# Performance work log

Hardware: AMD Instinct MI355X
Metric: run time of the kernel (lower is better)

Reference implementation:

```python
import jax, jax.numpy as jnp
import numpy as np

N = 10000            # nodes
E = 320000           # edges (avg degree 32)
L = 4                # layers
S = 64               # hidden 0e multiplicity
V = 16               # hidden 1o multiplicity
EMB = 32             # node-attr embedding dim
NB = 8               # bessel basis per channel (r and v -> 2*NB edge feats)
MR = 2.5             # max_radius
DEG = 32.0           # num_neighbors
GS = S + V           # gate input scalars: 64 scalars + 16 gates
NW = S * 2 + V * 2 + V * 2   # 192 per-edge tensor-product weights
MAXT = 100           # max atom types


def _semi_unitary(K):
    # Newton-Schulz orthogonalization: K^T K -> I (semi-unitary uplift matrix)
    K = K / jnp.linalg.norm(K)
    for _ in range(10):
        K = 1.5 * K - 0.5 * K @ (K.T @ K)
    return K


def _smooth_cutoff(t):
    u = 2.0 * (t - 1.0)
    y = (1.0 - jnp.cos(jnp.pi * u)) * 0.5
    return jnp.where(u > 0, 0.0, jnp.where(u < -1.0, 1.0, y))


def _edge_geom(d):
    # d: (E,3) edge vector. Returns cutoff-weighted 1x1o SH (component norm) and bessel features.
    r = jnp.linalg.norm(d, axis=1)                       # (E,)
    sh = np.sqrt(3.0) * d / r[:, None]                   # spherical harmonics 1x1o
    attr = _smooth_cutoff(r / MR)[:, None] * sh          # (E,3)
    k = jnp.arange(1, NB + 1, dtype=jnp.float32) * jnp.pi
    feat = np.sqrt(2.0 / MR) * jnp.sin(k * (r / MR)[:, None]) / r[:, None]
    return attr, feat * np.sqrt(NB)                      # (E,3), (E,NB)


def _fctp(s, v, attr, Ws, Wv):
    # FullyConnectedTensorProduct with pure-scalar (0e) node attr == attr-weighted per-irrep linear
    os = jnp.einsum('ni,ne,oie->no', s, attr, Ws) / np.sqrt(s.shape[1] * EMB)
    ov = jnp.einsum('nim,ne,oie->nom', v, attr, Wv) / np.sqrt(v.shape[1] * EMB)
    return os, ov


def _forward(x, node_attr, edge_src, edge_dst, emb_table, PU_K, h, mix,
             si_Ws, si_Wv, sc_Ws, sc_Wv, lin1_Ws, lin1_Wv, lin2_Ws, lin2_Wv,
             fc_W1, fc_b1, fc_W2, fc_b2, fc_W3, fc_b3):
    attr = emb_table[node_attr]                          # (N,EMB)
    K = _semi_unitary(PU_K)                              # (V,2)
    yv = jnp.einsum('ui,nim->num', K, x.reshape(N, 2, 3))  # uplift vectors
    ys = jnp.zeros((N, S), x.dtype)
    ys_old, yv_old = ys, yv
    c_s, c_x = np.sin(np.pi / 8), np.cos(np.pi / 8)
    for i in range(L):
        ar, fr = _edge_geom(x[:, :3][edge_src] - x[:, :3][edge_dst])
        av, fv = _edge_geom(x[:, 3:][edge_src] - x[:, 3:][edge_dst])
        a = jnp.stack([ar, av], axis=1)                  # (E,2,3) = 2x1o edge attr
        ef = jnp.concatenate([fr, fv], axis=1)           # (E,2*NB)
        # radial MLP -> per-edge TP weights
        hd = jax.nn.silu(ef @ fc_W1[i] + fc_b1[i])
        hd = jax.nn.silu(hd @ fc_W2[i] + fc_b2[i])
        w = hd @ fc_W3[i] + fc_b3[i]                     # (E,NW)
        w1 = w[:, :S * 2].reshape(-1, S, 2)
        w2 = w[:, S * 2:S * 2 + V * 2].reshape(-1, V, 2)
        w3 = w[:, S * 2 + V * 2:].reshape(-1, V, 2)
        # conv: lin1 -> gather -> TP -> scatter -> lin2 ; plus self-connection
        fs, fvv = _fctp(ys, yv, attr, lin1_Ws[i], lin1_Wv[i])
        s_src, v_src = fs[edge_src], fvv[edge_src]
        # 0e x 1o -> 1o (uvu)
        o1 = jnp.einsum('euv,eu,evm->eum', w1, s_src, a) / np.sqrt(2.0)   # (E,S,3)
        # 1o x 1o -> 0e (uvu)
        dots = jnp.einsum('eum,evm->euv', v_src, a)
        o2 = jnp.einsum('euv,euv->eu', w2, dots) / np.sqrt(6.0)           # (E,V)
        # 1o x 1o -> 1o (cross, uvu)
        cr = jnp.cross(v_src[:, :, None, :], a[:, None, :, :])            # (E,V,2,3)
        o3 = jnp.einsum('euv,euvm->eum', w3, cr) / 2.0                    # (E,V,3)
        mid_s = jax.ops.segment_sum(o2, edge_dst, num_segments=N) / np.sqrt(DEG)
        mid_v = jax.ops.segment_sum(jnp.concatenate([o1, o3], axis=1), edge_dst,
                                    num_segments=N) / np.sqrt(DEG)        # (N,S+V,3)
        cs2, cv2 = _fctp(mid_s, mid_v, attr, lin2_Ws[i], lin2_Wv[i])      # (N,GS),(N,V,3)
        scs, scv = _fctp(ys, yv, attr, sc_Ws[i], sc_Wv[i])
        conv_s = c_s * scs + c_x * cs2
        conv_v = c_s * scv + c_x * cv2
        # gate: silu scalars, sigmoid gates * gated vectors
        gns = jax.nn.silu(conv_s[:, :S])
        gnv = jax.nn.sigmoid(conv_s[:, S:])[:, :, None] * conv_v
        # self-interaction: per-irrep linear
        sis = ys @ si_Ws[i].T / np.sqrt(S)
        siv = jnp.einsum('oi,nim->nom', si_Wv[i], yv) / np.sqrt(V)
        # leapfrog update
        h2 = h[i] ** 2
        ns = 2.0 * ys - ys_old + h2 * (mix[i] * gns + (mix[i] - 1.0) * sis)
        nv = 2.0 * yv - yv_old + h2 * (mix[i] * gnv + (mix[i] - 1.0) * siv)
        ys_old, yv_old = ys, yv
        ys, yv = ns, nv
        x = jnp.einsum('ui,num->nim', K, yv).reshape(N, 6)   # project
    return x


def setup_inputs() -> dict:
    key = jax.random.key(0)
    ks = jax.random.split(key, 24)
    def g(i, sh, fan=1.0):
        return jax.random.normal(ks[i], sh, dtype=jnp.float32) / np.sqrt(fan)
    edge_src = jax.random.randint(ks[20], (E,), 0, N, dtype=jnp.int32)
    off = jax.random.randint(ks[21], (E,), 1, N, dtype=jnp.int32)
    edge_dst = (edge_src + off) % N                      # guarantees src != dst
    return {
        'x': g(0, (N, 6)),
        'batch': jnp.zeros((N,), jnp.int32),
        'node_attr': jax.random.randint(ks[22], (N,), 0, MAXT, dtype=jnp.int32),
        'edge_src': edge_src,
        'edge_dst': edge_dst,
        'emb_table': g(1, (MAXT, EMB)),
        'PU_K': g(2, (V, 2)),
        'h': jnp.full((L,), 0.01, jnp.float32),
        'mix': jnp.full((L,), 0.5, jnp.float32),
        'si_Ws': g(3, (L, S, S)), 'si_Wv': g(4, (L, V, V)),
        'sc_Ws': g(5, (L, GS, S, EMB)), 'sc_Wv': g(6, (L, V, V, EMB)),
        'lin1_Ws': g(7, (L, S, S, EMB)), 'lin1_Wv': g(8, (L, V, V, EMB)),
        'lin2_Ws': g(9, (L, GS, V, EMB)), 'lin2_Wv': g(10, (L, V, S + V, EMB)),
        'fc_W1': g(11, (L, 2 * NB, 64), 2 * NB), 'fc_b1': jnp.zeros((L, 64), jnp.float32),
        'fc_W2': g(12, (L, 64, 64), 64), 'fc_b2': jnp.zeros((L, 64), jnp.float32),
        'fc_W3': g(13, (L, 64, NW), 64), 'fc_b3': jnp.zeros((L, NW), jnp.float32),
    }


def reference(x, batch, node_attr, edge_src, edge_dst, emb_table, PU_K, h, mix,
              si_Ws, si_Wv, sc_Ws, sc_Wv, lin1_Ws, lin1_Wv, lin2_Ws, lin2_Wv,
              fc_W1, fc_b1, fc_W2, fc_b2, fc_W3, fc_b3):
    return _forward(x, node_attr, edge_src, edge_dst, emb_table, PU_K, h, mix,
                    si_Ws, si_Wv, sc_Ws, sc_Wv, lin1_Ws, lin1_Wv, lin2_Ws, lin2_Wv,
                    fc_W1, fc_b1, fc_W2, fc_b2, fc_W3, fc_b3)
```

## Files before the change

kernel.cpp:

```cpp
#include <hip/hip_runtime.h>
#include <hip/hip_fp8.h>
#include <math.h>

#define NN 10000
#define NE 320000
#define PI_F 3.14159265358979323846f

typedef __attribute__((ext_vector_type(8))) short short8x;
typedef __attribute__((ext_vector_type(4))) float float4x;
typedef __attribute__((ext_vector_type(4))) unsigned short ushort4x;

#if defined(__has_builtin)
#if __has_builtin(__builtin_amdgcn_cvt_pk_fp8_f32) && __has_builtin(__builtin_amdgcn_cvt_f32_fp8)
#define HW_FP8 1
#endif
#endif

__device__ __forceinline__ unsigned short f2b(float f) {
    unsigned b = __float_as_uint(f);
    return (unsigned short)((b + 0x7FFFu + ((b >> 16) & 1u)) >> 16);
}
__device__ __forceinline__ float b2f(unsigned short u) {
    return __uint_as_float(((unsigned)u) << 16);
}
__device__ __forceinline__ float silu(float x) {
    return x / (1.f + __expf(-x));
}
__device__ __forceinline__ unsigned char f2e4(float f) {
#ifdef HW_FP8
    int r = __builtin_amdgcn_cvt_pk_fp8_f32(f, f, 0, false);
    return (unsigned char)(r & 0xff);
#else
    __hip_fp8_e4m3 q(f);
    return (unsigned char)q.__x;
#endif
}
__device__ __forceinline__ float e42f(unsigned char v) {
#ifdef HW_FP8
    return __builtin_amdgcn_cvt_f32_fp8((int)v, 0);
#else
    __hip_fp8_e4m3 q;
    q.__x = (__hip_fp8_storage_t)v;
    return (float)q;
#endif
}
__device__ __forceinline__ float e4sel(unsigned word, int sel) {
#ifdef HW_FP8
    switch (sel & 3) {
        case 0:  return __builtin_amdgcn_cvt_f32_fp8((int)word, 0);
        case 1:  return __builtin_amdgcn_cvt_f32_fp8((int)word, 1);
        case 2:  return __builtin_amdgcn_cvt_f32_fp8((int)word, 2);
        default: return __builtin_amdgcn_cvt_f32_fp8((int)word, 3);
    }
#else
    return e42f((unsigned char)((word >> (8*(sel & 3))) & 0xffu));
#endif
}
__device__ __forceinline__ unsigned pk4(float a, float b, float c, float d) {
#ifdef HW_FP8
    unsigned w = (unsigned)__builtin_amdgcn_cvt_pk_fp8_f32(a, b, 0, false);
    w = (unsigned)__builtin_amdgcn_cvt_pk_fp8_f32(c, d, (int)w, true);
    return w;
#else
    return (unsigned)f2e4(a) | ((unsigned)f2e4(b) << 8) |
           ((unsigned)f2e4(c) << 16) | ((unsigned)f2e4(d) << 24);
#endif
}

__global__ void k_newton_kernel(const float* __restrict__ PU, float* __restrict__ Kout)
{
    if (threadIdx.x != 0 || blockIdx.x != 0) return;
    float K[32];
    float nrm = 0.f;
    for (int i = 0; i < 32; ++i) { K[i] = PU[i]; nrm += K[i]*K[i]; }
    float inv = 1.0f / sqrtf(nrm);
    for (int i = 0; i < 32; ++i) K[i] *= inv;
    for (int it = 0; it < 10; ++it) {
        float m00 = 0.f, m01 = 0.f, m11 = 0.f;
        for (int u = 0; u < 16; ++u) {
            float a = K[2*u], b = K[2*u+1];
            m00 += a*a; m01 += a*b; m11 += b*b;
        }
        for (int u = 0; u < 16; ++u) {
            float a = K[2*u], b = K[2*u+1];
            K[2*u]   = 1.5f*a - 0.5f*(a*m00 + b*m01);
            K[2*u+1] = 1.5f*b - 0.5f*(a*m01 + b*m11);
        }
    }
    for (int i = 0; i < 32; ++i) Kout[i] = K[i];
}

__global__ __launch_bounds__(256) void init_all_kernel(
    const float* __restrict__ x, const float* __restrict__ K,
    float* __restrict__ xp, float* __restrict__ yv0, float* __restrict__ yv1,
    float* __restrict__ ys0, float* __restrict__ ys1, float* __restrict__ fsb)
{
    int tid = blockIdx.x*256 + threadIdx.x;
    if (tid < NN*8) {
        int n = tid >> 3, c = tid & 7;
        xp[tid] = (c < 6) ? x[n*6 + c] : 0.f;
        return;
    }
    int t2 = tid - NN*8;
    if (t2 < NN*48) {
        int n = t2/48, j = t2%48, u = j/3, m = j%3;
        float v = K[2*u]*x[n*6+m] + K[2*u+1]*x[n*6+3+m];
        yv0[t2] = v; yv1[t2] = v;
        return;
    }
    t2 -= NN*48;
    if (t2 < NN*64) { ys0[t2] = 0.f; ys1[t2] = 0.f; fsb[t2] = 0.f; }
}

__global__ void init_fvv_kernel(const float* __restrict__ yv, const int* __restrict__ types,
                                const float* __restrict__ lin1vT0, float* __restrict__ fvv)
{
    int tid = blockIdx.x*blockDim.x + threadIdx.x;
    if (tid >= NN*48) return;
    int n = tid/48, j = tid%48, o = j/3, m = j%3;
    int t = types[n];
    const float* W = lin1vT0 + (size_t)t*256;
    float acc = 0.f;
    #pragma unroll
    for (int i = 0; i < 16; ++i) acc += yv[n*48 + i*3 + m]*W[i*16 + o];
    fvv[tid] = acc;
}

__device__ __forceinline__ void be_body(const float* __restrict__ W, const float* __restrict__ emb,
                                        float* __restrict__ out, int id, int O, int I, float scale)
{
    int o = id % O; int r = id / O;
    int i = r % I; r /= I;
    int t = r % 100; int l = r / 100;
    const float* w  = W + (((size_t)l*O + o)*I + i)*32;
    const float* em = emb + (size_t)t*32;
    float acc = 0.f;
    #pragma unroll
    for (int e = 0; e < 32; ++e) acc += w[e]*em[e];
    out[id] = acc*scale;
}

#define PREP_TOTAL (2048000 + 1638400 + 512000 + 512000 + 102400 + 102400 + 49152 + 16384 + 16384 + 8192 + 1024)
__global__ __launch_bounds__(256) void prep_kernel(
    const float* __restrict__ lin1_Ws, const float* __restrict__ lin1_Wv,
    const float* __restrict__ sc_Ws,   const float* __restrict__ sc_Wv,
    const float* __restrict__ lin2_Ws, const float* __restrict__ lin2_Wv,
    const float* __restrict__ si_Ws,   const float* __restrict__ si_Wv,
    const float* __restrict__ fc_W1,   const float* __restrict__ fc_W2,
    const float* __restrict__ fc_W3,   const float* __restrict__ emb,
    float* __restrict__ lin1sT, float* __restrict__ lin1vT,
    float* __restrict__ scsT,   float* __restrict__ scvT,
    float* __restrict__ lin2sT, float* __restrict__ lin2vT,
    float* __restrict__ siWsT,  float* __restrict__ siWvT,
    unsigned short* __restrict__ w1bp, unsigned short* __restrict__ w2bp,
    unsigned short* __restrict__ w3bf)
{
    const float s2048 = 0.022097086912079608f;
    const float s512  = 0.044194173824159216f;
    const float s2560 = 0.019764235376052372f;
    int tid = blockIdx.x*256 + threadIdx.x;
    if (tid < 2048000) { be_body(sc_Ws,   emb, scsT,   tid, 80, 64, s2048); return; }
    tid -= 2048000;
    if (tid < 1638400) { be_body(lin1_Ws, emb, lin1sT, tid, 64, 64, s2048); return; }
    tid -= 1638400;
    if (tid < 512000)  { be_body(lin2_Ws, emb, lin2sT, tid, 80, 16, s512);  return; }
    tid -= 512000;
    if (tid < 512000)  { be_body(lin2_Wv, emb, lin2vT, tid, 16, 80, s2560); return; }
    tid -= 512000;
    if (tid < 102400)  { be_body(lin1_Wv, emb, lin1vT, tid, 16, 16, s512);  return; }
    tid -= 102400;
    if (tid < 102400)  { be_body(sc_Wv,   emb, scvT,   tid, 16, 16, s512);  return; }
    tid -= 102400;
    if (tid < 49152) {
        int o = tid % 64; int r = tid / 64; int i = r % 192; int l = r / 192;
        w3bf[tid] = f2b(fc_W3[((size_t)l*64 + o)*192 + i]);
        return;
    }
    tid -= 49152;
    if (tid < 16384) {
        int o = tid % 64; int r = tid / 64; int i = r % 64; int l = r / 64;
        siWsT[tid] = si_Ws[((size_t)l*64 + o)*64 + i]*0.125f;
        return;
    }
    tid -= 16384;
    if (tid < 16384) {
        int kk = tid % 64; int r = tid / 64; int n = r % 64; int l = r / 64;
        w2bp[tid] = f2b(fc_W2[((size_t)l*64 + kk)*64 + n]);
        return;
    }
    tid -= 16384;
    if (tid < 8192) {
        int kk = tid % 32; int r = tid / 32; int n = r % 64; int l = r / 64;
        float v = (kk < 16) ? fc_W1[((size_t)l*16 + kk)*64 + n] : 0.f;
        w1bp[tid] = f2b(v);
        return;
    }
    tid -= 8192;
    if (tid < 1024) {
        int o = tid % 16; int r = tid / 16; int i = r % 16; int l = r / 16;
        siWvT[tid] = si_Wv[((size_t)l*16 + o)*16 + i]*0.25f;
    }
}

__global__ void hist_kernel(const int* __restrict__ dst, int* __restrict__ deg)
{
    int e = blockIdx.x*256 + threadIdx.x;
    if (e < NE) atomicAdd(&deg[dst[e]], 1);
}

__global__ __launch_bounds__(256) void scan_kernel(const int* __restrict__ deg,
                                                   int* __restrict__ segoff,
                                                   int* __restrict__ cursor)
{
    __shared__ int part[256];
    int tid = threadIdx.x;
    int base = tid*40;
    int s = 0;
    for (int i = 0; i < 40; ++i) { int idx = base+i; if (idx < NN) s += deg[idx]; }
    part[tid] = s;
    __syncthreads();
    for (int o = 1; o < 256; o <<= 1) {
        int v = (tid >= o) ? part[tid-o] : 0;
        __syncthreads();
        part[tid] += v;
        __syncthreads();
    }
    int excl = part[tid] - s;
    for (int i = 0; i < 40; ++i) {
        int idx = base+i;
        if (idx < NN) { segoff[idx] = excl; cursor[idx] = excl; excl += deg[idx]; }
        else if (idx == NN) { segoff[NN] = excl; }
    }
}

__global__ void scatter_kernel(const int* __restrict__ src, const int* __restrict__ dst,
                               int* __restrict__ cursor,
                               int* __restrict__ srcs, int* __restrict__ dsts)
{
    int e = blockIdx.x*256 + threadIdx.x;
    if (e >= NE) return;
    int d = dst[e];
    int p = atomicAdd(&cursor[d], 1);
    srcs[p] = src[e]; dsts[p] = d;
}

__global__ __launch_bounds__(256, 5) void edge_fused_kernel(
    const float* __restrict__ xp,
    const int* __restrict__ srcs, const int* __restrict__ dsts,
    const unsigned short* __restrict__ w1b,
    const float* __restrict__ b1,
    const unsigned short* __restrict__ w2b,
    const float* __restrict__ b2,
    const unsigned short* __restrict__ w3b,
    const float* __restrict__ b3,
    const float* __restrict__ fs, const float* __restrict__ fvv,
    float* __restrict__ mid)
{
    __shared__ __align__(16) unsigned char smem[192*68];
    __shared__ unsigned short fsl[64][68];
    __shared__ unsigned short fvl[48][68];
    __shared__ float abuf[6][68];
    __shared__ int sdst[64];
    __shared__ unsigned smaskl[2];
    unsigned short* hbuf = (unsigned short*)smem;
    const float C3f = 0.08838834764831845f;
    int lane = threadIdx.x & 63;
    int wid  = threadIdx.x >> 6;
    int eblk = blockIdx.x * 64;
    int row16 = lane & 15, quad = lane >> 4;
    int erow = 16*wid + row16;

    if (threadIdx.x < 64) {
        int tid = threadIdx.x;
        int own = dsts[eblk + tid];
        int pidx = eblk + tid - ((tid > 0) ? 1 : 0);
        int prev = dsts[pidx];
        sdst[tid] = own;
        bool nb = (tid > 0) && (own != prev);
        unsigned long long bm = __ballot(nb);
        if (tid == 0) { smaskl[0] = (unsigned)bm; smaskl[1] = (unsigned)(bm >> 32); }
    }

    if (lane < 32) {
        int eidx = 16*wid + (lane & 15);
        int half = lane >> 4;
        int p = eblk + eidx;
        int s = srcs[p], d = dsts[p];
        int off = 3*half;
        const float* xs = xp + (size_t)s*8 + off;
        const float* xd = xp + (size_t)d*8 + off;
        float d0 = xs[0]-xd[0], d1 = xs[1]-xd[1], d2 = xs[2]-xd[2];
        float r = sqrtf(d0*d0 + d1*d1 + d2*d2);
        float invr = 1.0f/r;
        float u = 0.8f*r - 2.0f;
        float cut = (u > 0.f) ? 0.f : ((u < -1.f) ? 1.f : 0.5f*(1.f - __cosf(PI_F*u)));
        float sc = 1.7320508075688772f*cut*invr;
        abuf[off+0][eidx] = sc*d0;
        abuf[off+1][eidx] = sc*d1;
        abuf[off+2][eidx] = sc*d2;
        float fsc = 2.5298221281347035f*invr;
        float wr = 1.2566370614359172f*r;
        unsigned epk[4];
        #pragma unroll
        for (int k = 0; k < 4; ++k) {
            float e0 = fsc*__sinf((float)(2*k+1)*wr);
            float e1 = fsc*__sinf((float)(2*k+2)*wr);
            epk[k] = (unsigned)f2b(e0) | ((unsigned)f2b(e1) << 16);
        }
        uint4* hr = (uint4*)(hbuf + eidx*72);
        uint4 q; q.x = epk[0]; q.y = epk[1]; q.z = epk[2]; q.w = epk[3];
        hr[half] = q;
        uint4 qz; qz.x = 0; qz.y = 0; qz.z = 0; qz.w = 0;
        hr[2+half] = qz;
    } else {
        int eidx = 16*wid + (lane & 15);
        int half = (lane >> 4) & 1;
        int s = srcs[eblk + eidx];
        const float4* fp = (const float4*)(fs + (size_t)s*64 + half*32);
        #pragma unroll
        for (int g = 0; g < 8; ++g) {
            float4 t = fp[g];
            int u0 = half*32 + g*4;
            fsl[u0+0][eidx] = f2b(t.x*0.125f);
            fsl[u0+1][eidx] = f2b(t.y*0.125f);
            fsl[u0+2][eidx] = f2b(t.z*0.125f);
            fsl[u0+3][eidx] = f2b(t.w*0.125f);
        }
        const float4* vp = (const float4*)(fvv + (size_t)s*48 + half*24);
        #pragma unroll
        for (int g = 0; g < 6; ++g) {
            float4 t = vp[g];
            int j0 = half*24 + g*4;
            fvl[j0+0][eidx] = f2b(t.x*C3f);
            fvl[j0+1][eidx] = f2b(t.y*C3f);
            fvl[j0+2][eidx] = f2b(t.z*C3f);
            fvl[j0+3][eidx] = f2b(t.w*C3f);
        }
    }

    {
        short8x a = *(const short8x*)(hbuf + erow*72 + quad*8);
        float4x c[4];
        #pragma unroll
        for (int nt = 0; nt < 4; ++nt) {
            short8x b = *(const short8x*)(w1b + ((size_t)(nt*16 + row16))*32 + quad*8);
            c[nt] = __builtin_amdgcn_mfma_f32_16x16x32_bf16(a, b, (float4x){0.f,0.f,0.f,0.f}, 0, 0, 0);
        }
        #pragma unroll
        for (int nt = 0; nt < 4; ++nt) {
            float bias = b1[nt*16 + row16];
            #pragma unroll
            for (int r = 0; r < 4; ++r) {
                float h = silu(c[nt][r] + bias);
                hbuf[(16*wid + quad*4 + r)*72 + nt*16 + row16] = f2b(h);
            }
        }
    }
    {
        short8x a0v = *(const short8x*)(hbuf + erow*72 + 0*32 + quad*8);
        short8x a1v = *(const short8x*)(hbuf + erow*72 + 1*32 + quad*8);
        float4x c[4];
        #pragma unroll
        for (int nt = 0; nt < 4; ++nt) {
            short8x b0 = *(const short8x*)(w2b + ((size_t)(nt*16 + row16))*64 + 0*32 + quad*8);
            float4x t = __builtin_amdgcn_mfma_f32_16x16x32_bf16(a0v, b0, (float4x){0.f,0.f,0.f,0.f}, 0, 0, 0);
            short8x b1v = *(const short8x*)(w2b + ((size_t)(nt*16 + row16))*64 + 1*32 + quad*8);
            c[nt] = __builtin_amdgcn_mfma_f32_16x16x32_bf16(a1v, b1v, t, 0, 0, 0);
        }
        #pragma unroll
        for (int nt = 0; nt < 4; ++nt) {
            float bias = b2[nt*16 + row16];
            #pragma unroll
            for (int r = 0; r < 4; ++r) {
                float h = silu(c[nt][r] + bias);
                hbuf[(16*wid + quad*4 + r)*72 + nt*16 + row16] = f2b(h);
            }
        }
    }
    {
        short8x a0v = *(const short8x*)(hbuf + erow*72 + 0*32 + quad*8);
        short8x a1v = *(const short8x*)(hbuf + erow*72 + 1*32 + quad*8);
        __syncthreads();
        float4x acc[12];
        #pragma unroll
        for (int nt = 0; nt < 12; ++nt) {
            short8x b0 = *(const short8x*)(w3b + ((size_t)(nt*16 + row16))*64 + 0*32 + quad*8);
            float4x t = __builtin_amdgcn_mfma_f32_16x16x32_bf16(a0v, b0, (float4x){0.f,0.f,0.f,0.f}, 0, 0, 0);
            short8x b1v = *(const short8x*)(w3b + ((size_t)(nt*16 + row16))*64 + 1*32 + quad*8);
            acc[nt] = __builtin_amdgcn_mfma_f32_16x16x32_bf16(a1v, b1v, t, 0, 0, 0);
        }
        #pragma unroll
        for (int nt = 0; nt < 12; ++nt) {
            unsigned pw = pk4(acc[nt][0], acc[nt][1], acc[nt][2], acc[nt][3]);
            *(unsigned*)(smem + (size_t)(nt*16 + row16)*68 + 16*wid + quad*4) = pw;
        }
    }
    __syncthreads();

    {
        unsigned mk0 = __builtin_amdgcn_readfirstlane(smaskl[0]);
        unsigned mk1 = __builtin_amdgcn_readfirstlane(smaskl[1]);
        bool iso1 = (wid < 2);
        int h = iso1 ? wid : (wid - 2);
        unsigned mkh = (h ? mk1 : mk0) & ~1u;
        int ebase = 32*h;
        int dcur = sdst[ebase];

        if (iso1) {
            const unsigned char* wp = smem + (size_t)(2*lane)*68;
            const unsigned short* fp = &fsl[lane][0];
            float bA = b3[2*lane], bB = b3[2*lane+1];
            float acc0 = 0.f, acc1 = 0.f, acc2 = 0.f;
            #pragma unroll
            for (int ch = 0; ch < 8; ++ch) {
                int e4 = ebase + 4*ch;
                unsigned wa4 = *(const unsigned*)(wp + e4);
                unsigned wb4 = *(const unsigned*)(wp + 68 + e4);
                ushort4x f4 = *(const ushort4x*)(fp + e4);
                float4x a00 = *(const float4x*)(&abuf[0][e4]);
                float4x a01 = *(const float4x*)(&abuf[1][e4]);
                float4x a02 = *(const float4x*)(&abuf[2][e4]);
                float4x a10 = *(const float4x*)(&abuf[3][e4]);
                float4x a11 = *(const float4x*)(&abuf[4][e4]);
                float4x a12 = *(const float4x*)(&abuf[5][e4]);
                float q0[4], q1[4], q2[4];
                #pragma unroll
                for (int k = 0; k < 4; ++k) {
                    float f = b2f(f4[k]);
                    float wa = (e4sel(wa4, k) + bA)*f;
                    float wb = (e4sel(wb4, k) + bB)*f;
                    q0[k] = wa*a00[k] + wb*a10[k];
                    q1[k] = wa*a01[k] + wb*a11[k];
                    q2[k] = wa*a02[k] + wb*a12[k];
                }
                unsigned mch = (mkh >> (4*ch)) & 15u;
                if (mch == 0) {
                    acc0 += (q0[0] + q0[1]) + (q0[2] + q0[3]);
                    acc1 += (q1[0] + q1[1]) + (q1[2] + q1[3]);
                    acc2 += (q2[0] + q2[1]) + (q2[2] + q2[3]);
                } else {
                    #pragma unroll
                    for (int k = 0; k < 4; ++k) {
                        if (mch & (1u << k)) {
                            float* mrow = mid + (size_t)dcur*256;
                            atomicAdd(mrow + 3*lane + 0, acc0);
                            atomicAdd(mrow + 3*lane + 1, acc1);
                            atomicAdd(mrow + 3*lane + 2, acc2);
                            acc0 = acc1 = acc2 = 0.f;
                            dcur = sdst[e4 + k];
                        }
                        acc0 += q0[k]; acc1 += q1[k]; acc2 += q2[k];
                    }
                }
            }
            float* mrow = mid + (size_t)dcur*256;
            atomicAdd(mrow + 3*lane + 0, acc0);
            atomicAdd(mrow + 3*lane + 1, acc1);
            atomicAdd(mrow + 3*lane + 2, acc2);
        } else {
            bool iso2 = lane < 16;
            int j3 = lane - 16;
            int u3 = j3 / 3;
            int m3 = j3 - 3*u3;
            int m1 = (m3 == 2) ? 0 : (m3 + 1);
            int m2 = 3 - m3 - m1;
            const unsigned char* wp;
            const unsigned short* vAp; const unsigned short* vBp; const unsigned short* vCp;
            const float* aX0; const float* aY0; const float* aZ0;
            const float* aX1; const float* aY1; const float* aZ1;
            float bA, bB, sgn, gam, FS;
            if (iso2) {
                wp = smem + (size_t)(128 + 2*lane)*68;
                bA = b3[128 + 2*lane]; bB = b3[129 + 2*lane];
                vAp = &fvl[3*lane+0][0]; vBp = &fvl[3*lane+1][0]; vCp = &fvl[3*lane+2][0];
                aX0 = &abuf[0][0]; aY0 = &abuf[1][0]; aZ0 = &abuf[2][0];
                aX1 = &abuf[3][0]; aY1 = &abuf[4][0]; aZ1 = &abuf[5][0];
                sgn = 1.f; gam = 1.f; FS = 0.8164965809277259f;
            } else {
                wp = smem + (size_t)(160 + 2*u3)*68;
                bA = b3[160 + 2*u3]; bB = b3[161 + 2*u3];
                vAp = &fvl[3*u3+m1][0]; vBp = &fvl[3*u3+m2][0]; vCp = &fvl[0][0];
                aX0 = &abuf[m2][0]; aY0 = &abuf[m1][0]; aZ0 = &abuf[0][0];
                aX1 = &abuf[3+m2][0]; aY1 = &abuf[3+m1][0]; aZ1 = &abuf[3][0];
                sgn = -1.f; gam = 0.f; FS = 1.f;
            }
            int cb = 192 + lane;
            float accb = 0.f;
            #pragma unroll
            for (int ch = 0; ch < 8; ++ch) {
                int e4 = ebase + 4*ch;
                unsigned wa4 = *(const unsigned*)(wp + e4);
                unsigned wb4 = *(const unsigned*)(wp + 68 + e4);
                ushort4x vA4 = *(const ushort4x*)(vAp + e4);
                ushort4x vB4 = *(const ushort4x*)(vBp + e4);
                ushort4x vC4 = *(const ushort4x*)(vCp + e4);
                float4x x0 = *(const float4x*)(aX0 + e4);
                float4x y0 = *(const float4x*)(aY0 + e4);
                float4x z0 = *(const float4x*)(aZ0 + e4);
                float4x x1 = *(const float4x*)(aX1 + e4);
                float4x y1 = *(const float4x*)(aY1 + e4);
                float4x z1 = *(const float4x*)(aZ1 + e4);
                float q[4];
                #pragma unroll
                for (int k = 0; k < 4; ++k) {
                    float fa = b2f(vA4[k]);
                    float fb = b2f(vB4[k]);
                    float fc = b2f(vC4[k]);
                    float dA = fmaf(sgn, fb*y0[k], fa*x0[k]);
                    dA = fmaf(gam, fc*z0[k], dA);
                    float dB = fmaf(sgn, fb*y1[k], fa*x1[k]);
                    dB = fmaf(gam, fc*z1[k], dB);
                    q[k] = (e4sel(wa4, k) + bA)*dA + (e4sel(wb4, k) + bB)*dB;
                }
                unsigned mch = (mkh >> (4*ch)) & 15u;
                if (mch == 0) {
                    accb += (q[0] + q[1]) + (q[2] + q[3]);
                } else {
                    #pragma unroll
                    for (int k = 0; k < 4; ++k) {
                        if (mch & (1u << k)) {
                            atomicAdd(mid + (size_t)dcur*256 + cb, accb*FS);
                            accb = 0.f;
                            dcur = sdst[e4 + k];
                        }
                        accb += q[k];
                    }
                }
            }
            atomicAdd(mid + (size_t)dcur*256 + cb, accb*FS);
        }
    }
}

__global__ __launch_bounds__(256) void node_update_kernel(
    const float* __restrict__ ys, const float* __restrict__ yv,
    float* __restrict__ ys_old, float* __restrict__ yv_old,
    const float* __restrict__ mid,
    const int* __restrict__ types,
    const float* __restrict__ scsT, const float* __restrict__ scvT,
    const float* __restrict__ lin2sT, const float* __restrict__ lin2vT,
    const float* __restrict__ siWsT, const float* __restrict__ siWvT,
    const float* __restrict__ lin1sTn, const float* __restrict__ lin1vTn,
    const float* __restrict__ Kbuf,
    const float* __restrict__ hv, const float* __restrict__ mixv, int layer,
    float* __restrict__ fs_out, float* __restrict__ fvv_out,
    float* __restrict__ xpad, float* __restrict__ dout)
{
    int n = blockIdx.x;
    int lane = threadIdx.x;
    __shared__ float ys_l[64], yv_l[48], mids[16], midv[240];
    __shared__ float conv_s[80], conv_v[48], sis_l[64], siv_l[48], ysn[64], yvn[48];
    int t = types[n];
    {
        float v = mid[(size_t)n*256 + lane];
        if (lane < 192) midv[lane] = v;
        else if (lane < 208) mids[lane-192] = v;
        else midv[192 + (lane-208)] = v;
    }
    if (lane < 64) ys_l[lane] = ys[n*64 + lane];
    else if (lane < 112) yv_l[lane-64] = yv[n*48 + (lane-64)];
    __syncthreads();
    if (lane < 80) {
        const float* Wsc = scsT + (size_t)t*5120;
        const float* W2s = lin2sT + (size_t)t*1280;
        float a_sc = 0.f, a_2 = 0.f;
        #pragma unroll
        for (int i = 0; i < 64; ++i) a_sc += ys_l[i]*Wsc[i*80 + lane];
        #pragma unroll
        for (int i = 0; i < 16; ++i) a_2 += mids[i]*W2s[i*80 + lane];
        conv_s[lane] = 0.3826834323650898f*a_sc + 0.9238795325112867f*a_2;
    } else if (lane < 144) {
        int o = lane - 80;
        float a_si = 0.f;
        #pragma unroll
        for (int i = 0; i < 64; ++i) a_si += ys_l[i]*siWsT[i*64 + o];
        sis_l[o] = a_si;
    } else if (lane < 192) {
        int j = lane - 144, o = j/3, m = j%3;
        const float* Wsc = scvT + (size_t)t*256;
        const float* W2v = lin2vT + (size_t)t*1280;
        float a_sc = 0.f, a_2 = 0.f, a_si = 0.f;
        #pragma unroll
        for (int i = 0; i < 16; ++i) {
            float y = yv_l[i*3+m];
            a_sc += y*Wsc[i*16+o];
            a_si += y*siWvT[i*16+o];
        }
        #pragma unroll
        for (int i = 0; i < 80; ++i) a_2 += midv[i*3+m]*W2v[i*16+o];
        conv_v[j] = 0.3826834323650898f*a_sc + 0.9238795325112867f*a_2;
        siv_l[j] = a_si;
    }
    __syncthreads();
    float hh = hv[layer]; float h2c = hh*hh; float mx = mixv[layer];
    if (lane < 64) {
        float cs = conv_s[lane];
        float gns = cs/(1.f + __expf(-cs));
        float ns = 2.f*ys_l[lane] - ys_old[n*64+lane] + h2c*(mx*gns + (mx-1.f)*sis_l[lane]);
        ys_old[n*64+lane] = ns;
        ysn[lane] = ns;
    } else if (lane < 112) {
        int j = lane-64, o = j/3;
        float g = 1.f/(1.f + __expf(-conv_s[64+o]));
        float gnv = g*conv_v[j];
        float nv = 2.f*yv_l[j] - yv_old[n*48+j] + h2c*(mx*gnv + (mx-1.f)*siv_l[j]);
        yv_old[n*48+j] = nv;
        yvn[j] = nv;
    }
    __syncthreads();
    if (lane < 6) {
        int i = lane/3, m = lane%3;
        float acc = 0.f;
        #pragma unroll
        for (int u = 0; u < 16; ++u) acc += Kbuf[2*u+i]*yvn[u*3+m];
        xpad[n*8 + lane] = acc;
        if (dout) dout[n*6 + lane] = acc;
    }
    if (lane < 64) {
        const float* W = lin1sTn + (size_t)t*4096;
        float acc = 0.f;
        #pragma unroll
        for (int i = 0; i < 64; ++i) acc += ysn[i]*W[i*64 + lane];
        fs_out[n*64 + lane] = acc;
    } else if (lane < 112) {
        int j = lane - 64, o = j/3, m = j%3;
        const float* W = lin1vTn + (size_t)t*256;
        float acc = 0.f;
        #pragma unroll
        for (int i = 0; i < 16; ++i) acc += yvn[i*3+m]*W[i*16 + o];
        fvv_out[n*48 + j] = acc;
    }
}

extern "C" void kernel_launch(void* const* d_in, const int* in_sizes, int n_in,
                              void* d_out, int out_size, void* d_ws, size_t ws_size,
                              hipStream_t stream)
{
    const float* x_in   = (const float*)d_in[0];
    const int*   types  = (const int*)  d_in[2];
    const int*   esrc   = (const int*)  d_in[3];
    const int*   edst   = (const int*)  d_in[4];
    const float* emb    = (const float*)d_in[5];
    const float* PU     = (const float*)d_in[6];
    const float* hv     = (const float*)d_in[7];
    const float* mixv   = (const float*)d_in[8];
    const float* si_Ws  = (const float*)d_in[9];
    const float* si_Wv  = (const float*)d_in[10];
    const float* sc_Ws  = (const float*)d_in[11];
    const float* sc_Wv  = (const float*)d_in[12];
    const float* lin1_Ws= (const float*)d_in[13];
    const float* lin1_Wv= (const float*)d_in[14];
    const float* lin2_Ws= (const float*)d_in[15];
    const float* lin2_Wv= (const float*)d_in[16];
    const float* fc_W1  = (const float*)d_in[17];
    const float* fc_b1  = (const float*)d_in[18];
    const float* fc_W2  = (const float*)d_in[19];
    const float* fc_b2  = (const float*)d_in[20];
    const float* fc_W3  = (const float*)d_in[21];
    const float* fc_b3  = (const float*)d_in[22];

    float* ws = (float*)d_ws;
    size_t off = 0;
    auto alloc = [&](size_t nf) { float* p = ws + off; off += nf; return p; };
    float* Kbuf   = alloc(64);
    float* x_pad  = alloc(80000);
    float* ys0    = alloc(640000);
    float* ys1    = alloc(640000);
    float* yv0    = alloc(480000);
    float* yv1    = alloc(480000);
    float* fsb    = alloc(640000);
    float* fvvb   = alloc(480000);
    float* midb   = alloc((size_t)NN*256);
    float* lin1sT = alloc((size_t)4*100*4096);
    float* lin1vT = alloc((size_t)4*100*256);
    float* scsT   = alloc((size_t)4*100*5120);
    float* scvT   = alloc((size_t)4*100*256);
    float* lin2sT = alloc((size_t)4*100*1280);
    float* lin2vT = alloc((size_t)4*100*1280);
    float* siWsT  = alloc((size_t)4*4096);
    float* siWvT  = alloc((size_t)4*256);
    int* iws = (int*)(ws + off);
    size_t ioff = 0;
    auto ialloc = [&](size_t ni) { int* p = iws + ioff; ioff += ni; return p; };
    int* deg    = ialloc(NN);
    int* segoff = ialloc(NN + 8);
    int* cursor = ialloc(NN);
    int* srcs   = ialloc(NE);
    int* dsts   = ialloc(NE);
    unsigned short* w1bp = (unsigned short*)(iws + ioff);
    unsigned short* w2bp = w1bp + (size_t)4*64*32;
    unsigned short* w3bf = w2bp + (size_t)4*64*64;

    k_newton_kernel<<<1, 1, 0, stream>>>(PU, Kbuf);
    prep_kernel<<<(PREP_TOTAL + 255)/256, 256, 0, stream>>>(
        lin1_Ws, lin1_Wv, sc_Ws, sc_Wv, lin2_Ws, lin2_Wv, si_Ws, si_Wv,
        fc_W1, fc_W2, fc_W3, emb,
        lin1sT, lin1vT, scsT, scvT, lin2sT, lin2vT, siWsT, siWvT,
        w1bp, w2bp, w3bf);
    {
        int tot = NN*8 + NN*48 + NN*64;
        init_all_kernel<<<(tot + 255)/256, 256, 0, stream>>>(
            x_in, Kbuf, x_pad, yv0, yv1, ys0, ys1, fsb);
    }
    init_fvv_kernel<<<(NN*48 + 255)/256, 256, 0, stream>>>(yv0, types, lin1vT, fvvb);

    (void)hipMemsetAsync(deg, 0, NN*sizeof(int), stream);
    hist_kernel<<<(NE+255)/256, 256, 0, stream>>>(edst, deg);
    scan_kernel<<<1, 256, 0, stream>>>(deg, segoff, cursor);
    scatter_kernel<<<(NE+255)/256, 256, 0, stream>>>(esrc, edst, cursor, srcs, dsts);

    float* ys_cur = ys0; float* ys_old = ys1;
    float* yv_cur = yv0; float* yv_old = yv1;
    for (int l = 0; l < 4; ++l) {
        (void)hipMemsetAsync(midb, 0, (size_t)NN*256*sizeof(float), stream);
        edge_fused_kernel<<<NE/64, 256, 0, stream>>>(
            x_pad, srcs, dsts,
            w1bp + (size_t)l*64*32,  fc_b1 + (size_t)l*64,
            w2bp + (size_t)l*64*64,  fc_b2 + (size_t)l*64,
            w3bf + (size_t)l*192*64, fc_b3 + (size_t)l*192,
            fsb, fvvb, midb);
        int ln = (l + 1) & 3;
        node_update_kernel<<<NN, 256, 0, stream>>>(
            ys_cur, yv_cur, ys_old, yv_old,
            midb, types,
            scsT   + (size_t)l*100*5120, scvT   + (size_t)l*100*256,
            lin2sT + (size_t)l*100*1280, lin2vT + (size_t)l*100*1280,
            siWsT  + (size_t)l*4096,     siWvT  + (size_t)l*256,
            lin1sT + (size_t)ln*100*4096, lin1vT + (size_t)ln*100*256,
            Kbuf, hv, mixv, l, fsb, fvvb,
            x_pad, (l == 3) ? (float*)d_out : nullptr);
        float* tmp;
        tmp = ys_cur; ys_cur = ys_old; ys_old = tmp;
        tmp = yv_cur; yv_cur = yv_old; yv_old = tmp;
    }
}
```

Baseline: 940.2 us.

## Read source node features directly from global memory instead of staging in LDS

Drops the LDS staging of per-edge source scalar and vector features (bf16-converted) and instead loads fp32 values from global memory inside the contraction loops, indexed by source ids cached in shared memory. The 1/8 and C3 scaling factors are folded into the final atomic adds and FS constants. This removes a prologue phase and about 15 KB of LDS per block, and the launch bounds are raised to allow more resident blocks. In exchange it issues many scattered global loads inside the inner loops, which may lean more on cache and add latency. Numerics shift slightly because the features are no longer rounded to bf16.

```diff
diff --git a/kernel.cpp b/kernel.cpp
--- a/kernel.cpp
+++ b/kernel.cpp
@@ -8,7 +8,6 @@
 
 typedef __attribute__((ext_vector_type(8))) short short8x;
 typedef __attribute__((ext_vector_type(4))) float float4x;
-typedef __attribute__((ext_vector_type(4))) unsigned short ushort4x;
 
 #if defined(__has_builtin)
 #if __has_builtin(__builtin_amdgcn_cvt_pk_fp8_f32) && __has_builtin(__builtin_amdgcn_cvt_f32_fp8)
@@ -244,7 +243,7 @@
     srcs[p] = src[e]; dsts[p] = d;
 }
 
-__global__ __launch_bounds__(256, 5) void edge_fused_kernel(
+__global__ __launch_bounds__(256, 6) void edge_fused_kernel(
     const float* __restrict__ xp,
     const int* __restrict__ srcs, const int* __restrict__ dsts,
     const unsigned short* __restrict__ w1b,
@@ -257,13 +256,10 @@
     float* __restrict__ mid)
 {
     __shared__ __align__(16) unsigned char smem[192*68];
-    __shared__ unsigned short fsl[64][68];
-    __shared__ unsigned short fvl[48][68];
     __shared__ float abuf[6][68];
-    __shared__ int sdst[64];
+    __shared__ int ssrc[64], sdst[64];
     __shared__ unsigned smaskl[2];
     unsigned short* hbuf = (unsigned short*)smem;
-    const float C3f = 0.08838834764831845f;
     int lane = threadIdx.x & 63;
     int wid  = threadIdx.x >> 6;
     int eblk = blockIdx.x * 64;
@@ -273,6 +269,7 @@
     if (threadIdx.x < 64) {
         int tid = threadIdx.x;
         int own = dsts[eblk + tid];
+        ssrc[tid] = srcs[eblk + tid];
         int pidx = eblk + tid - ((tid > 0) ? 1 : 0);
         int prev = dsts[pidx];
         sdst[tid] = own;
@@ -312,30 +309,6 @@
         hr[half] = q;
         uint4 qz; qz.x = 0; qz.y = 0; qz.z = 0; qz.w = 0;
         hr[2+half] = qz;
-    } else {
-        int eidx = 16*wid + (lane & 15);
-        int half = (lane >> 4) & 1;
-        int s = srcs[eblk + eidx];
-        const float4* fp = (const float4*)(fs + (size_t)s*64 + half*32);
-        #pragma unroll
-        for (int g = 0; g < 8; ++g) {
-            float4 t = fp[g];
-            int u0 = half*32 + g*4;
-            fsl[u0+0][eidx] = f2b(t.x*0.125f);
-            fsl[u0+1][eidx] = f2b(t.y*0.125f);
-            fsl[u0+2][eidx] = f2b(t.z*0.125f);
-            fsl[u0+3][eidx] = f2b(t.w*0.125f);
-        }
-        const float4* vp = (const float4*)(fvv + (size_t)s*48 + half*24);
-        #pragma unroll
-        for (int g = 0; g < 6; ++g) {
-            float4 t = vp[g];
-            int j0 = half*24 + g*4;
-            fvl[j0+0][eidx] = f2b(t.x*C3f);
-            fvl[j0+1][eidx] = f2b(t.y*C3f);
-            fvl[j0+2][eidx] = f2b(t.z*C3f);
-            fvl[j0+3][eidx] = f2b(t.w*C3f);
-        }
     }
 
     {
@@ -408,25 +381,29 @@
 
         if (iso1) {
             const unsigned char* wp = smem + (size_t)(2*lane)*68;
-            const unsigned short* fp = &fsl[lane][0];
             float bA = b3[2*lane], bB = b3[2*lane+1];
             float acc0 = 0.f, acc1 = 0.f, acc2 = 0.f;
             #pragma unroll
             for (int ch = 0; ch < 8; ++ch) {
                 int e4 = ebase + 4*ch;
+                int4 sv = *(const int4*)&ssrc[e4];
+                float f0 = fs[(size_t)sv.x*64 + lane];
+                float f1 = fs[(size_t)sv.y*64 + lane];
+                float f2 = fs[(size_t)sv.z*64 + lane];
+                float f3 = fs[(size_t)sv.w*64 + lane];
                 unsigned wa4 = *(const unsigned*)(wp + e4);
                 unsigned wb4 = *(const unsigned*)(wp + 68 + e4);
-                ushort4x f4 = *(const ushort4x*)(fp + e4);
                 float4x a00 = *(const float4x*)(&abuf[0][e4]);
                 float4x a01 = *(const float4x*)(&abuf[1][e4]);
                 float4x a02 = *(const float4x*)(&abuf[2][e4]);
                 float4x a10 = *(const float4x*)(&abuf[3][e4]);
                 float4x a11 = *(const float4x*)(&abuf[4][e4]);
                 float4x a12 = *(const float4x*)(&abuf[5][e4]);
+                float fv[4] = {f0, f1, f2, f3};
                 float q0[4], q1[4], q2[4];
                 #pragma unroll
                 for (int k = 0; k < 4; ++k) {
-                    float f = b2f(f4[k]);
+                    float f = fv[k];
                     float wa = (e4sel(wa4, k) + bA)*f;
                     float wb = (e4sel(wb4, k) + bB)*f;
                     q0[k] = wa*a00[k] + wb*a10[k];
@@ -443,9 +420,9 @@
                     for (int k = 0; k < 4; ++k) {
                         if (mch & (1u << k)) {
                             float* mrow = mid + (size_t)dcur*256;
-                            atomicAdd(mrow + 3*lane + 0, acc0);
-                            atomicAdd(mrow + 3*lane + 1, acc1);
-                            atomicAdd(mrow + 3*lane + 2, acc2);
+                            atomicAdd(mrow + 3*lane + 0, acc0*0.125f);
+                            atomicAdd(mrow + 3*lane + 1, acc1*0.125f);
+                            atomicAdd(mrow + 3*lane + 2, acc2*0.125f);
                             acc0 = acc1 = acc2 = 0.f;
                             dcur = sdst[e4 + k];
                         }
@@ -454,9 +431,9 @@
                 }
             }
             float* mrow = mid + (size_t)dcur*256;
-            atomicAdd(mrow + 3*lane + 0, acc0);
-            atomicAdd(mrow + 3*lane + 1, acc1);
-            atomicAdd(mrow + 3*lane + 2, acc2);
+            atomicAdd(mrow + 3*lane + 0, acc0*0.125f);
+            atomicAdd(mrow + 3*lane + 1, acc1*0.125f);
+            atomicAdd(mrow + 3*lane + 2, acc2*0.125f);
         } else {
             bool iso2 = lane < 16;
             int j3 = lane - 16;
@@ -465,47 +442,58 @@
             int m1 = (m3 == 2) ? 0 : (m3 + 1);
             int m2 = 3 - m3 - m1;
             const unsigned char* wp;
-            const unsigned short* vAp; const unsigned short* vBp; const unsigned short* vCp;
+            int rA, rB, rC;
             const float* aX0; const float* aY0; const float* aZ0;
             const float* aX1; const float* aY1; const float* aZ1;
             float bA, bB, sgn, gam, FS;
             if (iso2) {
                 wp = smem + (size_t)(128 + 2*lane)*68;
                 bA = b3[128 + 2*lane]; bB = b3[129 + 2*lane];
-                vAp = &fvl[3*lane+0][0]; vBp = &fvl[3*lane+1][0]; vCp = &fvl[3*lane+2][0];
+                rA = 3*lane; rB = 3*lane + 1; rC = 3*lane + 2;
                 aX0 = &abuf[0][0]; aY0 = &abuf[1][0]; aZ0 = &abuf[2][0];
                 aX1 = &abuf[3][0]; aY1 = &abuf[4][0]; aZ1 = &abuf[5][0];
-                sgn = 1.f; gam = 1.f; FS = 0.8164965809277259f;
+                sgn = 1.f; gam = 1.f; FS = 0.07216878364870323f;
             } else {
                 wp = smem + (size_t)(160 + 2*u3)*68;
                 bA = b3[160 + 2*u3]; bB = b3[161 + 2*u3];
-                vAp = &fvl[3*u3+m1][0]; vBp = &fvl[3*u3+m2][0]; vCp = &fvl[0][0];
+                rA = 3*u3 + m1; rB = 3*u3 + m2; rC = 0;
                 aX0 = &abuf[m2][0]; aY0 = &abuf[m1][0]; aZ0 = &abuf[0][0];
                 aX1 = &abuf[3+m2][0]; aY1 = &abuf[3+m1][0]; aZ1 = &abuf[3][0];
-                sgn = -1.f; gam = 0.f; FS = 1.f;
+                sgn = -1.f; gam = 0.f; FS = 0.08838834764831845f;
             }
             int cb = 192 + lane;
             float accb = 0.f;
             #pragma unroll
             for (int ch = 0; ch < 8; ++ch) {
                 int e4 = ebase + 4*ch;
+                int4 sv = *(const int4*)&ssrc[e4];
+                float fa0 = fvv[(size_t)sv.x*48 + rA];
+                float fb0 = fvv[(size_t)sv.x*48 + rB];
+                float fc0 = fvv[(size_t)sv.x*48 + rC];
+                float fa1 = fvv[(size_t)sv.y*48 + rA];
+                float fb1 = fvv[(size_t)sv.y*48 + rB];
+                float fc1 = fvv[(size_t)sv.y*48 + rC];
+                float fa2 = fvv[(size_t)sv.z*48 + rA];
+                float fb2 = fvv[(size_t)sv.z*48 + rB];
+                float fc2 = fvv[(size_t)sv.z*48 + rC];
+                float fa3 = fvv[(size_t)sv.w*48 + rA];
+                float fb3 = fvv[(size_t)sv.w*48 + rB];
+                float fc3 = fvv[(size_t)sv.w*48 + rC];
                 unsigned wa4 = *(const unsigned*)(wp + e4);
                 unsigned wb4 = *(const unsigned*)(wp + 68 + e4);
-                ushort4x vA4 = *(const ushort4x*)(vAp + e4);
-                ushort4x vB4 = *(const ushort4x*)(vBp + e4);
-                ushort4x vC4 = *(const ushort4x*)(vCp + e4);
                 float4x x0 = *(const float4x*)(aX0 + e4);
                 float4x y0 = *(const float4x*)(aY0 + e4);
                 float4x z0 = *(const float4x*)(aZ0 + e4);
                 float4x x1 = *(const float4x*)(aX1 + e4);
                 float4x y1 = *(const float4x*)(aY1 + e4);
                 float4x z1 = *(const float4x*)(aZ1 + e4);
+                float fav[4] = {fa0, fa1, fa2, fa3};
+                float fbv[4] = {fb0, fb1, fb2, fb3};
+                float fcv[4] = {fc0, fc1, fc2, fc3};
                 float q[4];
                 #pragma unroll
                 for (int k = 0; k < 4; ++k) {
-                    float fa = b2f(vA4[k]);
-                    float fb = b2f(vB4[k]);
-                    float fc = b2f(vC4[k]);
+                    float fa = fav[k], fb = fbv[k], fc = fcv[k];
                     float dA = fmaf(sgn, fb*y0[k], fa*x0[k]);
                     dA = fmaf(gam, fc*z0[k], dA);
                     float dB = fmaf(sgn, fb*y1[k], fa*x1[k]);
```

Result: no change. 950.6 us (+1.1%).
